# Optimization experiments

Hardware: AMD Instinct MI355X
Metric: run time of the kernel (lower is better)

## Reference

```python
import jax, jax.numpy as jnp
import numpy as np

B, H, W, D = 64, 32, 32, 64
K = 1024  # codebook_size


def setup_inputs() -> dict:
    key = jax.random.key(0)
    kz, ke = jax.random.split(key)
    z = jax.random.normal(kz, (B, H, W, D), dtype=jnp.float32)
    embeddings = 0.02 * jax.random.normal(ke, (K, D), dtype=jnp.float32)
    return {"z": z, "embeddings": embeddings}


def reference(z, embeddings):
    # Flatten spatial/batch dims: (N, D) with N = B*H*W
    z_flat = z.reshape(-1, z.shape[-1])
    # Squared euclidean distances via ||a||^2 + ||b||^2 - 2 a.b  -> (N, K)
    distances = (jnp.sum(z_flat ** 2, axis=1, keepdims=True)
                 + jnp.sum(embeddings ** 2, axis=1)
                 - 2.0 * jnp.dot(z_flat, embeddings.T))
    indices = jnp.argmin(distances, axis=1)  # (N,)
    quantized = embeddings[indices].reshape(z.shape)  # (B, H, W, D)
    indices = indices.reshape(z.shape[0], z.shape[1], z.shape[2])  # (B, H, W)
    return quantized, indices
```

## Files before the change

### kernel.cpp

```cpp
#include <hip/hip_runtime.h>

#define NPTS   65536
#define DDIM   64
#define KCODES 1024
#define QOUT_ELEMS (NPTS * DDIM)

typedef _Float16 half8    __attribute__((ext_vector_type(8)));
typedef float    floatx16 __attribute__((ext_vector_type(16)));
typedef unsigned int uint;

#define AS1 __attribute__((address_space(1)))
#define AS3 __attribute__((address_space(3)))

#define WS_EHP   0
#define WS_ELP   (128*1024)
#define WS_E2    (256*1024)

union H8U { half8 v; uint u[4]; };

static __device__ __forceinline__ void gl_lds16(const void* g, void* l) {
    __builtin_amdgcn_global_load_lds((const AS1 uint*)g, (AS3 uint*)l, 16, 0, 0);
}

__global__ void eprep_kernel(const float* __restrict__ emb, char* __restrict__ ws) {
    const int tid = threadIdx.x;
    const int w = tid >> 6, d = tid & 63;
    const int k = blockIdx.x * 4 + w;
    float v = emb[(size_t)k * DDIM + d];
    _Float16 h = (_Float16)v;
    _Float16 l = (_Float16)(v - (float)h);
    size_t off = (size_t)(k >> 5) * 4096 + (size_t)(d >> 3) * 512
               + (size_t)(k & 31) * 16 + (size_t)(d & 7) * 2;
    *(_Float16*)(ws + WS_EHP + off) = h;
    *(_Float16*)(ws + WS_ELP + off) = l;
    float s = v * v;
    #pragma unroll
    for (int m = 1; m < 64; m <<= 1) s += __shfl_xor(s, m, 64);
    if (d == 0) {
        _Float16 e2h = (_Float16)s;
        _Float16 e2l = (_Float16)(s - (float)e2h);
        unsigned short hb = *(unsigned short*)&e2h;
        unsigned short lb = *(unsigned short*)&e2l;
        ((uint*)(ws + WS_E2))[k] = (uint)hb | ((uint)lb << 16);
    }
}

__global__ __launch_bounds__(256, 3) void vq_kernel(
    const float* __restrict__ z,
    const char* __restrict__ ws_c,
    const float* __restrict__ emb,
    float* __restrict__ out)
{
    const int tid  = threadIdx.x;
    const int lane = tid & 63;
    const int w    = __builtin_amdgcn_readfirstlane(tid >> 6);
    const int col  = lane & 31;
    const int sel8 = lane >> 5;
    const int pgrp = blockIdx.x;

    __shared__ uint4 ldseh[256];
    __shared__ uint4 ldsel[256];
    __shared__ uint  lds_e2[1024];
    __shared__ int   s_final[128];

    const int pt = pgrp * 128 + w * 32 + col;
    half8 ah[4], al[4];
    {
        const float* zrow = z + (size_t)pt * DDIM + sel8 * 8;
        #pragma unroll
        for (int ks = 0; ks < 4; ++ks) {
            float4 u0 = *(const float4*)(zrow + ks * 16);
            float4 u1 = *(const float4*)(zrow + ks * 16 + 4);
            float tv[8] = {u0.x, u0.y, u0.z, u0.w, u1.x, u1.y, u1.z, u1.w};
            #pragma unroll
            for (int j = 0; j < 8; ++j) {
                float a = -2.0f * tv[j];
                _Float16 hh = (_Float16)a;
                ah[ks][j] = hh;
                al[ks][j] = (_Float16)(a - (float)hh);
            }
        }
    }
    half8 ahE;
    { H8U t0; t0.u[0] = (sel8 == 0) ? 0x3C003C00u : 0u;
      t0.u[1] = t0.u[2] = t0.u[3] = 0u; ahE = t0.v; }

    gl_lds16(ws_c + WS_E2 + w * 1024 + lane * 16, (char*)lds_e2 + w * 1024);

    const floatx16 zeroC = {};

    float best[16];
    int   bt[16];
    #pragma unroll
    for (int r = 0; r < 16; ++r) { best[r] = 3.4e38f; bt[r] = 0; }

    const int myoff = sel8 * 512 + col * 16;

    for (int t = 0; t < 32; ++t) {
        __syncthreads();
        {
            const int opnd = w >> 1, half = w & 1;
            const char* src = ws_c + (opnd ? WS_ELP : WS_EHP)
                            + (size_t)t * 4096 + half * 2048 + lane * 16;
            char* dst = (char*)(opnd ? ldsel : ldseh) + half * 2048;
            gl_lds16(src, dst);
            gl_lds16(src + 1024, dst + 1024);
        }
        __syncthreads();

        const char* ehb = (const char*)ldseh + myoff;
        const char* elb = (const char*)ldsel + myoff;
        half8 bh[4], bl[4];
        #pragma unroll
        for (int ks = 0; ks < 4; ++ks) {
            bh[ks] = *(const half8*)(ehb + ks * 1024);
            bl[ks] = *(const half8*)(elb + ks * 1024);
        }
        half8 bhE;
        { H8U u; u.u[0] = lds_e2[t * 32 + col];
          u.u[1] = u.u[2] = u.u[3] = 0u; bhE = u.v; }

        floatx16 acc = __builtin_amdgcn_mfma_f32_32x32x16_f16(ah[0], bh[0], zeroC, 0, 0, 0);
        acc = __builtin_amdgcn_mfma_f32_32x32x16_f16(ah[1], bh[1], acc, 0, 0, 0);
        acc = __builtin_amdgcn_mfma_f32_32x32x16_f16(ah[2], bh[2], acc, 0, 0, 0);
        acc = __builtin_amdgcn_mfma_f32_32x32x16_f16(ah[3], bh[3], acc, 0, 0, 0);
        acc = __builtin_amdgcn_mfma_f32_32x32x16_f16(ahE,  bhE,  acc, 0, 0, 0);
        acc = __builtin_amdgcn_mfma_f32_32x32x16_f16(ah[0], bl[0], acc, 0, 0, 0);
        acc = __builtin_amdgcn_mfma_f32_32x32x16_f16(ah[1], bl[1], acc, 0, 0, 0);
        acc = __builtin_amdgcn_mfma_f32_32x32x16_f16(ah[2], bl[2], acc, 0, 0, 0);
        acc = __builtin_amdgcn_mfma_f32_32x32x16_f16(ah[3], bl[3], acc, 0, 0, 0);
        acc = __builtin_amdgcn_mfma_f32_32x32x16_f16(al[0], bh[0], acc, 0, 0, 0);
        acc = __builtin_amdgcn_mfma_f32_32x32x16_f16(al[1], bh[1], acc, 0, 0, 0);
        acc = __builtin_amdgcn_mfma_f32_32x32x16_f16(al[2], bh[2], acc, 0, 0, 0);
        acc = __builtin_amdgcn_mfma_f32_32x32x16_f16(al[3], bh[3], acc, 0, 0, 0);

        #pragma unroll
        for (int r = 0; r < 16; ++r) {
            bool c = acc[r] < best[r];
            best[r] = c ? acc[r] : best[r];
            bt[r]   = c ? t      : bt[r];
        }
    }

    int code[16];
    #pragma unroll
    for (int r = 0; r < 16; ++r) code[r] = bt[r] * 32 + col;
    #pragma unroll
    for (int m = 1; m < 32; m <<= 1) {
        #pragma unroll
        for (int r = 0; r < 16; ++r) {
            float ov = __shfl_xor(best[r], m, 64);
            int   oc = __shfl_xor(code[r], m, 64);
            bool c = (ov < best[r]) || (ov == best[r] && oc < code[r]);
            best[r] = c ? ov : best[r];
            code[r] = c ? oc : code[r];
        }
    }
    if (col == 0) {
        #pragma unroll
        for (int r = 0; r < 16; ++r) {
            int row = (r & 3) + 8 * (r >> 2) + 4 * sel8;
            s_final[w * 32 + row] = code[r];
        }
    }
    __syncthreads();

    if (tid < 128)
        out[QOUT_ELEMS + (size_t)pgrp * 128 + tid] = (float)s_final[tid];
    float4* outq = (float4*)out;
    const float4* emb4 = (const float4*)emb;
    #pragma unroll
    for (int it = 0; it < 8; ++it) {
        int f  = it * 256 + tid;
        int p  = f >> 4;
        int d4 = f & 15;
        int ks = s_final[p];
        outq[((size_t)pgrp * 128 + p) * (DDIM / 4) + d4] =
            emb4[(size_t)ks * (DDIM / 4) + d4];
    }
}

extern "C" void kernel_launch(void* const* d_in, const int* in_sizes, int n_in,
                              void* d_out, int out_size, void* d_ws, size_t ws_size,
                              hipStream_t stream) {
    const float* z   = (const float*)d_in[0];
    const float* emb = (const float*)d_in[1];
    float* out = (float*)d_out;
    char* ws = (char*)d_ws;

    eprep_kernel<<<KCODES / 4, 256, 0, stream>>>(emb, ws);
    vq_kernel<<<NPTS / 128, 256, 0, stream>>>(z, ws, emb, out);
}
```

Baseline: 102.0 us.

## Split codebook across blocks, double-buffer LDS, add separate merge-gather kernel

Each block now handles 256 points (two 32-row sets per wave) against half the codebook, so every B fragment loaded from LDS feeds two MFMA chains. Codebook tiles are double-buffered in LDS with prefetch, which removes one barrier per iteration. Partial argmins go to a workspace scratch buffer, and a new merge kernel picks between the two halves and does the embedding gather. The cost is a third kernel launch, the scratch round-trip, higher register pressure, and occupancy lowered from 3 to 2 blocks.

```diff
diff --git a/kernel.cpp b/kernel.cpp
--- a/kernel.cpp
+++ b/kernel.cpp
@@ -15,6 +15,7 @@
 #define WS_EHP   0
 #define WS_ELP   (128*1024)
 #define WS_E2    (256*1024)
+#define WS_SCR   (264*1024)
 
 union H8U { half8 v; uint u[4]; };
 
@@ -45,27 +46,26 @@
     }
 }
 
-__global__ __launch_bounds__(256, 3) void vq_kernel(
+__global__ __launch_bounds__(256, 2) void vq_kernel(
     const float* __restrict__ z,
     const char* __restrict__ ws_c,
-    const float* __restrict__ emb,
-    float* __restrict__ out)
+    float2* __restrict__ scr)
 {
     const int tid  = threadIdx.x;
     const int lane = tid & 63;
     const int w    = __builtin_amdgcn_readfirstlane(tid >> 6);
     const int col  = lane & 31;
     const int sel8 = lane >> 5;
-    const int pgrp = blockIdx.x;
-
-    __shared__ uint4 ldseh[256];
-    __shared__ uint4 ldsel[256];
-    __shared__ uint  lds_e2[1024];
-    __shared__ int   s_final[128];
-
-    const int pt = pgrp * 128 + w * 32 + col;
-    half8 ah[4], al[4];
-    {
+    const int pgrp  = blockIdx.x >> 1;
+    const int khalf = blockIdx.x & 1;
+
+    __shared__ uint4 ldsbuf[2][1024];
+    __shared__ uint  lds_e2[512];
+
+    half8 ah[2][4], al[2][4];
+    #pragma unroll
+    for (int set = 0; set < 2; ++set) {
+        const int pt = pgrp * 256 + w * 64 + set * 32 + col;
         const float* zrow = z + (size_t)pt * DDIM + sel8 * 8;
         #pragma unroll
         for (int ks = 0; ks < 4; ++ks) {
@@ -76,8 +76,8 @@
             for (int j = 0; j < 8; ++j) {
                 float a = -2.0f * tv[j];
                 _Float16 hh = (_Float16)a;
-                ah[ks][j] = hh;
-                al[ks][j] = (_Float16)(a - (float)hh);
+                ah[set][ks][j] = hh;
+                al[set][ks][j] = (_Float16)(a - (float)hh);
             }
         }
     }
@@ -85,99 +85,136 @@
     { H8U t0; t0.u[0] = (sel8 == 0) ? 0x3C003C00u : 0u;
       t0.u[1] = t0.u[2] = t0.u[3] = 0u; ahE = t0.v; }
 
-    gl_lds16(ws_c + WS_E2 + w * 1024 + lane * 16, (char*)lds_e2 + w * 1024);
+    if (w < 2)
+        gl_lds16(ws_c + WS_E2 + khalf * 2048 + w * 1024 + lane * 16,
+                 (char*)lds_e2 + w * 1024);
+    {
+        const int opnd = w >> 1, q = w & 1;
+        const char* src = ws_c + (opnd ? WS_ELP : WS_EHP)
+                        + (size_t)(khalf * 16 + q) * 4096 + lane * 16;
+        char* dst = (char*)ldsbuf[0] + (opnd * 8192 + q * 4096);
+        #pragma unroll
+        for (int i = 0; i < 4; ++i)
+            gl_lds16(src + i * 1024, dst + i * 1024);
+    }
 
     const floatx16 zeroC = {};
-
-    float best[16];
-    int   bt[16];
-    #pragma unroll
-    for (int r = 0; r < 16; ++r) { best[r] = 3.4e38f; bt[r] = 0; }
-
-    const int myoff = sel8 * 512 + col * 16;
-
-    for (int t = 0; t < 32; ++t) {
+    float best[2][16];
+    int   bt[2][16];
+    #pragma unroll
+    for (int set = 0; set < 2; ++set)
+        #pragma unroll
+        for (int r = 0; r < 16; ++r) { best[set][r] = 3.4e38f; bt[set][r] = 0; }
+
+    for (int s = 0; s < 8; ++s) {
         __syncthreads();
-        {
-            const int opnd = w >> 1, half = w & 1;
+        if (s < 7) {
+            const int opnd = w >> 1, q = w & 1;
             const char* src = ws_c + (opnd ? WS_ELP : WS_EHP)
-                            + (size_t)t * 4096 + half * 2048 + lane * 16;
-            char* dst = (char*)(opnd ? ldsel : ldseh) + half * 2048;
-            gl_lds16(src, dst);
-            gl_lds16(src + 1024, dst + 1024);
-        }
-        __syncthreads();
-
-        const char* ehb = (const char*)ldseh + myoff;
-        const char* elb = (const char*)ldsel + myoff;
-        half8 bh[4], bl[4];
-        #pragma unroll
-        for (int ks = 0; ks < 4; ++ks) {
-            bh[ks] = *(const half8*)(ehb + ks * 1024);
-            bl[ks] = *(const half8*)(elb + ks * 1024);
-        }
-        half8 bhE;
-        { H8U u; u.u[0] = lds_e2[t * 32 + col];
-          u.u[1] = u.u[2] = u.u[3] = 0u; bhE = u.v; }
-
-        floatx16 acc = __builtin_amdgcn_mfma_f32_32x32x16_f16(ah[0], bh[0], zeroC, 0, 0, 0);
-        acc = __builtin_amdgcn_mfma_f32_32x32x16_f16(ah[1], bh[1], acc, 0, 0, 0);
-        acc = __builtin_amdgcn_mfma_f32_32x32x16_f16(ah[2], bh[2], acc, 0, 0, 0);
-        acc = __builtin_amdgcn_mfma_f32_32x32x16_f16(ah[3], bh[3], acc, 0, 0, 0);
-        acc = __builtin_amdgcn_mfma_f32_32x32x16_f16(ahE,  bhE,  acc, 0, 0, 0);
-        acc = __builtin_amdgcn_mfma_f32_32x32x16_f16(ah[0], bl[0], acc, 0, 0, 0);
-        acc = __builtin_amdgcn_mfma_f32_32x32x16_f16(ah[1], bl[1], acc, 0, 0, 0);
-        acc = __builtin_amdgcn_mfma_f32_32x32x16_f16(ah[2], bl[2], acc, 0, 0, 0);
-        acc = __builtin_amdgcn_mfma_f32_32x32x16_f16(ah[3], bl[3], acc, 0, 0, 0);
-        acc = __builtin_amdgcn_mfma_f32_32x32x16_f16(al[0], bh[0], acc, 0, 0, 0);
-        acc = __builtin_amdgcn_mfma_f32_32x32x16_f16(al[1], bh[1], acc, 0, 0, 0);
-        acc = __builtin_amdgcn_mfma_f32_32x32x16_f16(al[2], bh[2], acc, 0, 0, 0);
-        acc = __builtin_amdgcn_mfma_f32_32x32x16_f16(al[3], bh[3], acc, 0, 0, 0);
-
-        #pragma unroll
-        for (int r = 0; r < 16; ++r) {
-            bool c = acc[r] < best[r];
-            best[r] = c ? acc[r] : best[r];
-            bt[r]   = c ? t      : bt[r];
-        }
-    }
-
-    int code[16];
-    #pragma unroll
-    for (int r = 0; r < 16; ++r) code[r] = bt[r] * 32 + col;
-    #pragma unroll
-    for (int m = 1; m < 32; m <<= 1) {
-        #pragma unroll
-        for (int r = 0; r < 16; ++r) {
-            float ov = __shfl_xor(best[r], m, 64);
-            int   oc = __shfl_xor(code[r], m, 64);
-            bool c = (ov < best[r]) || (ov == best[r] && oc < code[r]);
-            best[r] = c ? ov : best[r];
-            code[r] = c ? oc : code[r];
-        }
-    }
-    if (col == 0) {
-        #pragma unroll
-        for (int r = 0; r < 16; ++r) {
-            int row = (r & 3) + 8 * (r >> 2) + 4 * sel8;
-            s_final[w * 32 + row] = code[r];
-        }
-    }
-    __syncthreads();
-
-    if (tid < 128)
-        out[QOUT_ELEMS + (size_t)pgrp * 128 + tid] = (float)s_final[tid];
-    float4* outq = (float4*)out;
-    const float4* emb4 = (const float4*)emb;
-    #pragma unroll
-    for (int it = 0; it < 8; ++it) {
-        int f  = it * 256 + tid;
-        int p  = f >> 4;
-        int d4 = f & 15;
-        int ks = s_final[p];
-        outq[((size_t)pgrp * 128 + p) * (DDIM / 4) + d4] =
-            emb4[(size_t)ks * (DDIM / 4) + d4];
-    }
+                            + (size_t)(khalf * 16 + (s + 1) * 2 + q) * 4096 + lane * 16;
+            char* dst = (char*)ldsbuf[(s + 1) & 1] + (opnd * 8192 + q * 4096);
+            #pragma unroll
+            for (int i = 0; i < 4; ++i)
+                gl_lds16(src + i * 1024, dst + i * 1024);
+        }
+        const char* buf = (const char*)ldsbuf[s & 1];
+
+        #pragma unroll
+        for (int q = 0; q < 2; ++q) {
+            const int tg = s * 2 + q;
+            const char* ehb = buf + q * 4096 + sel8 * 512 + col * 16;
+            const char* elb = ehb + 8192;
+            half8 bh[4], bl[4];
+            #pragma unroll
+            for (int ks = 0; ks < 4; ++ks) {
+                bh[ks] = *(const half8*)(ehb + ks * 1024);
+                bl[ks] = *(const half8*)(elb + ks * 1024);
+            }
+            half8 bhE;
+            { H8U u; u.u[0] = lds_e2[tg * 32 + col];
+              u.u[1] = u.u[2] = u.u[3] = 0u; bhE = u.v; }
+
+            floatx16 a0, a1;
+            a0 = __builtin_amdgcn_mfma_f32_32x32x16_f16(ah[0][0], bh[0], zeroC, 0, 0, 0);
+            a1 = __builtin_amdgcn_mfma_f32_32x32x16_f16(ah[1][0], bh[0], zeroC, 0, 0, 0);
+            a0 = __builtin_amdgcn_mfma_f32_32x32x16_f16(ah[0][1], bh[1], a0, 0, 0, 0);
+            a1 = __builtin_amdgcn_mfma_f32_32x32x16_f16(ah[1][1], bh[1], a1, 0, 0, 0);
+            a0 = __builtin_amdgcn_mfma_f32_32x32x16_f16(ah[0][2], bh[2], a0, 0, 0, 0);
+            a1 = __builtin_amdgcn_mfma_f32_32x32x16_f16(ah[1][2], bh[2], a1, 0, 0, 0);
+            a0 = __builtin_amdgcn_mfma_f32_32x32x16_f16(ah[0][3], bh[3], a0, 0, 0, 0);
+            a1 = __builtin_amdgcn_mfma_f32_32x32x16_f16(ah[1][3], bh[3], a1, 0, 0, 0);
+            a0 = __builtin_amdgcn_mfma_f32_32x32x16_f16(ahE, bhE, a0, 0, 0, 0);
+            a1 = __builtin_amdgcn_mfma_f32_32x32x16_f16(ahE, bhE, a1, 0, 0, 0);
+            a0 = __builtin_amdgcn_mfma_f32_32x32x16_f16(ah[0][0], bl[0], a0, 0, 0, 0);
+            a1 = __builtin_amdgcn_mfma_f32_32x32x16_f16(ah[1][0], bl[0], a1, 0, 0, 0);
+            a0 = __builtin_amdgcn_mfma_f32_32x32x16_f16(ah[0][1], bl[1], a0, 0, 0, 0);
+            a1 = __builtin_amdgcn_mfma_f32_32x32x16_f16(ah[1][1], bl[1], a1, 0, 0, 0);
+            a0 = __builtin_amdgcn_mfma_f32_32x32x16_f16(ah[0][2], bl[2], a0, 0, 0, 0);
+            a1 = __builtin_amdgcn_mfma_f32_32x32x16_f16(ah[1][2], bl[2], a1, 0, 0, 0);
+            a0 = __builtin_amdgcn_mfma_f32_32x32x16_f16(ah[0][3], bl[3], a0, 0, 0, 0);
+            a1 = __builtin_amdgcn_mfma_f32_32x32x16_f16(ah[1][3], bl[3], a1, 0, 0, 0);
+            a0 = __builtin_amdgcn_mfma_f32_32x32x16_f16(al[0][0], bh[0], a0, 0, 0, 0);
+            a1 = __builtin_amdgcn_mfma_f32_32x32x16_f16(al[1][0], bh[0], a1, 0, 0, 0);
+            a0 = __builtin_amdgcn_mfma_f32_32x32x16_f16(al[0][1], bh[1], a0, 0, 0, 0);
+            a1 = __builtin_amdgcn_mfma_f32_32x32x16_f16(al[1][1], bh[1], a1, 0, 0, 0);
+            a0 = __builtin_amdgcn_mfma_f32_32x32x16_f16(al[0][2], bh[2], a0, 0, 0, 0);
+            a1 = __builtin_amdgcn_mfma_f32_32x32x16_f16(al[1][2], bh[2], a1, 0, 0, 0);
+            a0 = __builtin_amdgcn_mfma_f32_32x32x16_f16(al[0][3], bh[3], a0, 0, 0, 0);
+            a1 = __builtin_amdgcn_mfma_f32_32x32x16_f16(al[1][3], bh[3], a1, 0, 0, 0);
+
+            #pragma unroll
+            for (int r = 0; r < 16; ++r) {
+                bool c0 = a0[r] < best[0][r];
+                best[0][r] = c0 ? a0[r] : best[0][r];
+                bt[0][r]   = c0 ? tg    : bt[0][r];
+                bool c1 = a1[r] < best[1][r];
+                best[1][r] = c1 ? a1[r] : best[1][r];
+                bt[1][r]   = c1 ? tg    : bt[1][r];
+            }
+        }
+    }
+
+    #pragma unroll
+    for (int set = 0; set < 2; ++set) {
+        int code[16];
+        #pragma unroll
+        for (int r = 0; r < 16; ++r)
+            code[r] = khalf * 512 + bt[set][r] * 32 + col;
+        #pragma unroll
+        for (int m = 1; m < 32; m <<= 1) {
+            #pragma unroll
+            for (int r = 0; r < 16; ++r) {
+                float ov = __shfl_xor(best[set][r], m, 64);
+                int   oc = __shfl_xor(code[r], m, 64);
+                bool c = (ov < best[set][r]) || (ov == best[set][r] && oc < code[r]);
+                best[set][r] = c ? ov : best[set][r];
+                code[r]      = c ? oc : code[r];
+            }
+        }
+        if (col == 0) {
+            #pragma unroll
+            for (int r = 0; r < 16; ++r) {
+                int row = (r & 3) + 8 * (r >> 2) + 4 * sel8;
+                int p = pgrp * 256 + w * 64 + set * 32 + row;
+                scr[(size_t)p * 2 + khalf] =
+                    make_float2(best[set][r], __int_as_float(code[r]));
+            }
+        }
+    }
+}
+
+__global__ void merge_gather_kernel(const float* __restrict__ emb,
+                                    const float2* __restrict__ scr,
+                                    float* __restrict__ out)
+{
+    int f = blockIdx.x * 256 + threadIdx.x;
+    int pt = f >> 4, d4 = f & 15;
+    float2 c0 = scr[(size_t)pt * 2];
+    float2 c1 = scr[(size_t)pt * 2 + 1];
+    int i0 = __float_as_int(c0.y), i1 = __float_as_int(c1.y);
+    int idx = (c1.x < c0.x) ? i1 : i0;
+    ((float4*)out)[(size_t)pt * 16 + d4] = ((const float4*)emb)[(size_t)idx * 16 + d4];
+    if (d4 == 0) out[QOUT_ELEMS + pt] = (float)idx;
 }
 
 extern "C" void kernel_launch(void* const* d_in, const int* in_sizes, int n_in,
@@ -187,7 +224,9 @@
     const float* emb = (const float*)d_in[1];
     float* out = (float*)d_out;
     char* ws = (char*)d_ws;
+    float2* scr = (float2*)(ws + WS_SCR);
 
     eprep_kernel<<<KCODES / 4, 256, 0, stream>>>(emb, ws);
-    vq_kernel<<<NPTS / 128, 256, 0, stream>>>(z, ws, emb, out);
-}
+    vq_kernel<<<512, 256, 0, stream>>>(z, ws, scr);
+    merge_gather_kernel<<<NPTS * 16 / 256, 256, 0, stream>>>(emb, scr, out);
+}
```

After: 111.7 us. 1.1x slower.

## Split codebook across 4 blocks per point group with double-buffered LDS and merge kernel

Applied to the files above, without the earlier changes.

Each point group of 128 points is now handled by four blocks, each scanning a quarter of the codebook. That quadruples the grid from 512 to 2048 blocks to fill more CUs. Codebook tiles are double-buffered in LDS, issuing the next tile's load before the current compute, which removes one barrier per iteration. Each block writes partial (best distance, index) pairs to workspace, and a new merge_gather kernel picks the minimum and gathers the embedding rows. The cost is an extra launch, a scratch round-trip, and the z loads and conversion repeated four times. Tie-breaking in the merge keeps the earlier quarter on equal distances, which preserves lowest-index semantics.

```diff
diff --git a/kernel.cpp b/kernel.cpp
--- a/kernel.cpp
+++ b/kernel.cpp
@@ -15,6 +15,7 @@
 #define WS_EHP   0
 #define WS_ELP   (128*1024)
 #define WS_E2    (256*1024)
+#define WS_SCR   (264*1024)
 
 union H8U { half8 v; uint u[4]; };
 
@@ -48,20 +49,18 @@
 __global__ __launch_bounds__(256, 3) void vq_kernel(
     const float* __restrict__ z,
     const char* __restrict__ ws_c,
-    const float* __restrict__ emb,
-    float* __restrict__ out)
+    float2* __restrict__ scr)
 {
     const int tid  = threadIdx.x;
     const int lane = tid & 63;
     const int w    = __builtin_amdgcn_readfirstlane(tid >> 6);
     const int col  = lane & 31;
     const int sel8 = lane >> 5;
-    const int pgrp = blockIdx.x;
-
-    __shared__ uint4 ldseh[256];
-    __shared__ uint4 ldsel[256];
-    __shared__ uint  lds_e2[1024];
-    __shared__ int   s_final[128];
+    const int pgrp = blockIdx.x >> 2;
+    const int kq   = blockIdx.x & 3;
+
+    __shared__ uint4 ldsbuf[2][512];
+    __shared__ uint  lds_e2[256];
 
     const int pt = pgrp * 128 + w * 32 + col;
     half8 ah[4], al[4];
@@ -85,31 +84,36 @@
     { H8U t0; t0.u[0] = (sel8 == 0) ? 0x3C003C00u : 0u;
       t0.u[1] = t0.u[2] = t0.u[3] = 0u; ahE = t0.v; }
 
-    gl_lds16(ws_c + WS_E2 + w * 1024 + lane * 16, (char*)lds_e2 + w * 1024);
+    if (w == 0)
+        gl_lds16(ws_c + WS_E2 + kq * 1024 + lane * 16, (char*)lds_e2);
+    {
+        const int opnd = w >> 1, hf = w & 1;
+        const char* src = ws_c + (opnd ? WS_ELP : WS_EHP)
+                        + (size_t)(kq * 8) * 4096 + hf * 2048 + lane * 16;
+        char* dst = (char*)ldsbuf[0] + opnd * 4096 + hf * 2048;
+        gl_lds16(src, dst);
+        gl_lds16(src + 1024, dst + 1024);
+    }
 
     const floatx16 zeroC = {};
-
     float best[16];
     int   bt[16];
     #pragma unroll
     for (int r = 0; r < 16; ++r) { best[r] = 3.4e38f; bt[r] = 0; }
 
-    const int myoff = sel8 * 512 + col * 16;
-
-    for (int t = 0; t < 32; ++t) {
+    for (int t = 0; t < 8; ++t) {
         __syncthreads();
-        {
-            const int opnd = w >> 1, half = w & 1;
+        if (t < 7) {
+            const int opnd = w >> 1, hf = w & 1;
             const char* src = ws_c + (opnd ? WS_ELP : WS_EHP)
-                            + (size_t)t * 4096 + half * 2048 + lane * 16;
-            char* dst = (char*)(opnd ? ldsel : ldseh) + half * 2048;
+                            + (size_t)(kq * 8 + t + 1) * 4096 + hf * 2048 + lane * 16;
+            char* dst = (char*)ldsbuf[(t + 1) & 1] + opnd * 4096 + hf * 2048;
             gl_lds16(src, dst);
             gl_lds16(src + 1024, dst + 1024);
         }
-        __syncthreads();
-
-        const char* ehb = (const char*)ldseh + myoff;
-        const char* elb = (const char*)ldsel + myoff;
+        const char* buf = (const char*)ldsbuf[t & 1];
+        const char* ehb = buf + sel8 * 512 + col * 16;
+        const char* elb = ehb + 4096;
         half8 bh[4], bl[4];
         #pragma unroll
         for (int ks = 0; ks < 4; ++ks) {
@@ -120,7 +124,8 @@
         { H8U u; u.u[0] = lds_e2[t * 32 + col];
           u.u[1] = u.u[2] = u.u[3] = 0u; bhE = u.v; }
 
-        floatx16 acc = __builtin_amdgcn_mfma_f32_32x32x16_f16(ah[0], bh[0], zeroC, 0, 0, 0);
+        floatx16 acc;
+        acc = __builtin_amdgcn_mfma_f32_32x32x16_f16(ah[0], bh[0], zeroC, 0, 0, 0);
         acc = __builtin_amdgcn_mfma_f32_32x32x16_f16(ah[1], bh[1], acc, 0, 0, 0);
         acc = __builtin_amdgcn_mfma_f32_32x32x16_f16(ah[2], bh[2], acc, 0, 0, 0);
         acc = __builtin_amdgcn_mfma_f32_32x32x16_f16(ah[3], bh[3], acc, 0, 0, 0);
@@ -144,7 +149,7 @@
 
     int code[16];
     #pragma unroll
-    for (int r = 0; r < 16; ++r) code[r] = bt[r] * 32 + col;
+    for (int r = 0; r < 16; ++r) code[r] = kq * 256 + bt[r] * 32 + col;
     #pragma unroll
     for (int m = 1; m < 32; m <<= 1) {
         #pragma unroll
@@ -160,24 +165,27 @@
         #pragma unroll
         for (int r = 0; r < 16; ++r) {
             int row = (r & 3) + 8 * (r >> 2) + 4 * sel8;
-            s_final[w * 32 + row] = code[r];
-        }
-    }
-    __syncthreads();
-
-    if (tid < 128)
-        out[QOUT_ELEMS + (size_t)pgrp * 128 + tid] = (float)s_final[tid];
-    float4* outq = (float4*)out;
-    const float4* emb4 = (const float4*)emb;
-    #pragma unroll
-    for (int it = 0; it < 8; ++it) {
-        int f  = it * 256 + tid;
-        int p  = f >> 4;
-        int d4 = f & 15;
-        int ks = s_final[p];
-        outq[((size_t)pgrp * 128 + p) * (DDIM / 4) + d4] =
-            emb4[(size_t)ks * (DDIM / 4) + d4];
-    }
+            int p = pgrp * 128 + w * 32 + row;
+            scr[(size_t)p * 4 + kq] = make_float2(best[r], __int_as_float(code[r]));
+        }
+    }
+}
+
+__global__ void merge_gather_kernel(const float* __restrict__ emb,
+                                    const float2* __restrict__ scr,
+                                    float* __restrict__ out)
+{
+    int f = blockIdx.x * 256 + threadIdx.x;
+    int pt = f >> 4, d4 = f & 15;
+    float2 c0 = scr[(size_t)pt * 4];
+    float bv = c0.x; int bi = __float_as_int(c0.y);
+    #pragma unroll
+    for (int j = 1; j < 4; ++j) {
+        float2 cj = scr[(size_t)pt * 4 + j];
+        if (cj.x < bv) { bv = cj.x; bi = __float_as_int(cj.y); }
+    }
+    ((float4*)out)[(size_t)pt * 16 + d4] = ((const float4*)emb)[(size_t)bi * 16 + d4];
+    if (d4 == 0) out[QOUT_ELEMS + pt] = (float)bi;
 }
 
 extern "C" void kernel_launch(void* const* d_in, const int* in_sizes, int n_in,
@@ -187,7 +195,9 @@
     const float* emb = (const float*)d_in[1];
     float* out = (float*)d_out;
     char* ws = (char*)d_ws;
+    float2* scr = (float2*)(ws + WS_SCR);
 
     eprep_kernel<<<KCODES / 4, 256, 0, stream>>>(emb, ws);
-    vq_kernel<<<NPTS / 128, 256, 0, stream>>>(z, ws, emb, out);
-}
+    vq_kernel<<<2048, 256, 0, stream>>>(z, ws, scr);
+    merge_gather_kernel<<<NPTS * 16 / 256, 256, 0, stream>>>(emb, scr, out);
+}
```

After: 118.0 us. 1.16x slower.

## Use single-wave blocks with register double-buffered codebook loads from global memory

Applied to the files above, without the earlier changes.

Replaces the 4-wave block that staged codebook tiles through LDS with barriers with 64-thread single-wave blocks. Each wave loads B-operand tiles straight from global memory (L2-cached) into registers, double-buffered so the next tile's load overlaps the current tile's MFMAs. The ||e||^2 term is now added in fp32 after the MFMAs instead of through an extra MFMA. The gather epilogue is also done per wave without LDS. This removes the barriers and the LDS traffic, but every wave now re-reads the whole codebook from global/L2, which raises cache bandwidth pressure.

```diff
diff --git a/kernel.cpp b/kernel.cpp
--- a/kernel.cpp
+++ b/kernel.cpp
@@ -9,18 +9,9 @@
 typedef float    floatx16 __attribute__((ext_vector_type(16)));
 typedef unsigned int uint;
 
-#define AS1 __attribute__((address_space(1)))
-#define AS3 __attribute__((address_space(3)))
-
 #define WS_EHP   0
 #define WS_ELP   (128*1024)
-#define WS_E2    (256*1024)
-
-union H8U { half8 v; uint u[4]; };
-
-static __device__ __forceinline__ void gl_lds16(const void* g, void* l) {
-    __builtin_amdgcn_global_load_lds((const AS1 uint*)g, (AS3 uint*)l, 16, 0, 0);
-}
+#define WS_E2F   (256*1024)
 
 __global__ void eprep_kernel(const float* __restrict__ emb, char* __restrict__ ws) {
     const int tid = threadIdx.x;
@@ -36,37 +27,58 @@
     float s = v * v;
     #pragma unroll
     for (int m = 1; m < 64; m <<= 1) s += __shfl_xor(s, m, 64);
-    if (d == 0) {
-        _Float16 e2h = (_Float16)s;
-        _Float16 e2l = (_Float16)(s - (float)e2h);
-        unsigned short hb = *(unsigned short*)&e2h;
-        unsigned short lb = *(unsigned short*)&e2l;
-        ((uint*)(ws + WS_E2))[k] = (uint)hb | ((uint)lb << 16);
-    }
+    if (d == 0) ((float*)(ws + WS_E2F))[k] = s;
 }
 
-__global__ __launch_bounds__(256, 3) void vq_kernel(
+#define MFMA __builtin_amdgcn_mfma_f32_32x32x16_f16
+
+#define LOAD_TILE(BH, BL, E2V, tt) do {                                       \
+    const char* _p = ws_c + WS_EHP + (size_t)(tt) * 4096 + sel8 * 512 + col * 16; \
+    _Pragma("unroll") for (int _k = 0; _k < 4; ++_k)                          \
+        BH[_k] = *(const half8*)(_p + _k * 1024);                             \
+    _Pragma("unroll") for (int _k = 0; _k < 4; ++_k)                          \
+        BL[_k] = *(const half8*)(_p + (WS_ELP - WS_EHP) + _k * 1024);         \
+    E2V = e2f[(tt) * 32 + col];                                               \
+} while (0)
+
+#define DO_TILE(BH, BL, E2V, TCUR) do {                                       \
+    floatx16 acc;                                                             \
+    acc = MFMA(ah[0], BH[0], zeroC, 0, 0, 0);                                 \
+    acc = MFMA(ah[1], BH[1], acc, 0, 0, 0);                                   \
+    acc = MFMA(ah[2], BH[2], acc, 0, 0, 0);                                   \
+    acc = MFMA(ah[3], BH[3], acc, 0, 0, 0);                                   \
+    acc = MFMA(ah[0], BL[0], acc, 0, 0, 0);                                   \
+    acc = MFMA(ah[1], BL[1], acc, 0, 0, 0);                                   \
+    acc = MFMA(ah[2], BL[2], acc, 0, 0, 0);                                   \
+    acc = MFMA(ah[3], BL[3], acc, 0, 0, 0);                                   \
+    acc = MFMA(al[0], BH[0], acc, 0, 0, 0);                                   \
+    acc = MFMA(al[1], BH[1], acc, 0, 0, 0);                                   \
+    acc = MFMA(al[2], BH[2], acc, 0, 0, 0);                                   \
+    acc = MFMA(al[3], BH[3], acc, 0, 0, 0);                                   \
+    const int vcode = (TCUR) * 32 + col;                                      \
+    _Pragma("unroll") for (int _r = 0; _r < 16; ++_r) {                       \
+        float _s = acc[_r] + (E2V);                                           \
+        bool _c = _s < best[_r];        \
+        best[_r]  = _c ? _s    : best[_r];                                    \
+        bcode[_r] = _c ? vcode : bcode[_r];                                   \
+    }                                                                         \
+} while (0)
+
+__global__ __launch_bounds__(64, 2) void vq_kernel(
     const float* __restrict__ z,
     const char* __restrict__ ws_c,
     const float* __restrict__ emb,
     float* __restrict__ out)
 {
-    const int tid  = threadIdx.x;
-    const int lane = tid & 63;
-    const int w    = __builtin_amdgcn_readfirstlane(tid >> 6);
+    const int lane = threadIdx.x & 63;
     const int col  = lane & 31;
     const int sel8 = lane >> 5;
-    const int pgrp = blockIdx.x;
+    const int ptbase = blockIdx.x * 32;
+    const float* e2f = (const float*)(ws_c + WS_E2F);
 
-    __shared__ uint4 ldseh[256];
-    __shared__ uint4 ldsel[256];
-    __shared__ uint  lds_e2[1024];
-    __shared__ int   s_final[128];
-
-    const int pt = pgrp * 128 + w * 32 + col;
     half8 ah[4], al[4];
     {
-        const float* zrow = z + (size_t)pt * DDIM + sel8 * 8;
+        const float* zrow = z + (size_t)(ptbase + col) * DDIM + sel8 * 8;
         #pragma unroll
         for (int ks = 0; ks < 4; ++ks) {
             float4 u0 = *(const float4*)(zrow + ks * 16);
@@ -81,102 +93,44 @@
             }
         }
     }
-    half8 ahE;
-    { H8U t0; t0.u[0] = (sel8 == 0) ? 0x3C003C00u : 0u;
-      t0.u[1] = t0.u[2] = t0.u[3] = 0u; ahE = t0.v; }
-
-    gl_lds16(ws_c + WS_E2 + w * 1024 + lane * 16, (char*)lds_e2 + w * 1024);
 
     const floatx16 zeroC = {};
+    float best[16];
+    int   bcode[16];
+    #pragma unroll
+    for (int r = 0; r < 16; ++r) { best[r] = 3.4e38f; bcode[r] = 0; }
 
-    float best[16];
-    int   bt[16];
-    #pragma unroll
-    for (int r = 0; r < 16; ++r) { best[r] = 3.4e38f; bt[r] = 0; }
-
-    const int myoff = sel8 * 512 + col * 16;
-
-    for (int t = 0; t < 32; ++t) {
-        __syncthreads();
-        {
-            const int opnd = w >> 1, half = w & 1;
-            const char* src = ws_c + (opnd ? WS_ELP : WS_EHP)
-                            + (size_t)t * 4096 + half * 2048 + lane * 16;
-            char* dst = (char*)(opnd ? ldsel : ldseh) + half * 2048;
-            gl_lds16(src, dst);
-            gl_lds16(src + 1024, dst + 1024);
-        }
-        __syncthreads();
-
-        const char* ehb = (const char*)ldseh + myoff;
-        const char* elb = (const char*)ldsel + myoff;
-        half8 bh[4], bl[4];
-        #pragma unroll
-        for (int ks = 0; ks < 4; ++ks) {
-            bh[ks] = *(const half8*)(ehb + ks * 1024);
-            bl[ks] = *(const half8*)(elb + ks * 1024);
-        }
-        half8 bhE;
-        { H8U u; u.u[0] = lds_e2[t * 32 + col];
-          u.u[1] = u.u[2] = u.u[3] = 0u; bhE = u.v; }
-
-        floatx16 acc = __builtin_amdgcn_mfma_f32_32x32x16_f16(ah[0], bh[0], zeroC, 0, 0, 0);
-        acc = __builtin_amdgcn_mfma_f32_32x32x16_f16(ah[1], bh[1], acc, 0, 0, 0);
-        acc = __builtin_amdgcn_mfma_f32_32x32x16_f16(ah[2], bh[2], acc, 0, 0, 0);
-        acc = __builtin_amdgcn_mfma_f32_32x32x16_f16(ah[3], bh[3], acc, 0, 0, 0);
-        acc = __builtin_amdgcn_mfma_f32_32x32x16_f16(ahE,  bhE,  acc, 0, 0, 0);
-        acc = __builtin_amdgcn_mfma_f32_32x32x16_f16(ah[0], bl[0], acc, 0, 0, 0);
-        acc = __builtin_amdgcn_mfma_f32_32x32x16_f16(ah[1], bl[1], acc, 0, 0, 0);
-        acc = __builtin_amdgcn_mfma_f32_32x32x16_f16(ah[2], bl[2], acc, 0, 0, 0);
-        acc = __builtin_amdgcn_mfma_f32_32x32x16_f16(ah[3], bl[3], acc, 0, 0, 0);
-        acc = __builtin_amdgcn_mfma_f32_32x32x16_f16(al[0], bh[0], acc, 0, 0, 0);
-        acc = __builtin_amdgcn_mfma_f32_32x32x16_f16(al[1], bh[1], acc, 0, 0, 0);
-        acc = __builtin_amdgcn_mfma_f32_32x32x16_f16(al[2], bh[2], acc, 0, 0, 0);
-        acc = __builtin_amdgcn_mfma_f32_32x32x16_f16(al[3], bh[3], acc, 0, 0, 0);
-
-        #pragma unroll
-        for (int r = 0; r < 16; ++r) {
-            bool c = acc[r] < best[r];
-            best[r] = c ? acc[r] : best[r];
-            bt[r]   = c ? t      : bt[r];
-        }
+    half8 b0h[4], b0l[4], b1h[4], b1l[4];
+    float e20, e21;
+    LOAD_TILE(b0h, b0l, e20, 0);
+    for (int t = 0; t < 32; t += 2) {
+        LOAD_TILE(b1h, b1l, e21, t + 1);
+        DO_TILE(b0h, b0l, e20, t);
+        const int t2 = (t + 2 < 32) ? t + 2 : 31;
+        LOAD_TILE(b0h, b0l, e20, t2);
+        DO_TILE(b1h, b1l, e21, t + 1);
     }
 
-    int code[16];
-    #pragma unroll
-    for (int r = 0; r < 16; ++r) code[r] = bt[r] * 32 + col;
     #pragma unroll
     for (int m = 1; m < 32; m <<= 1) {
         #pragma unroll
         for (int r = 0; r < 16; ++r) {
-            float ov = __shfl_xor(best[r], m, 64);
-            int   oc = __shfl_xor(code[r], m, 64);
-            bool c = (ov < best[r]) || (ov == best[r] && oc < code[r]);
-            best[r] = c ? ov : best[r];
-            code[r] = c ? oc : code[r];
+            float ov = __shfl_xor(best[r],  m, 64);
+            int   oc = __shfl_xor(bcode[r], m, 64);
+            bool c = (ov < best[r]) || (ov == best[r] && oc < bcode[r]);
+            best[r]  = c ? ov : best[r];
+            bcode[r] = c ? oc : bcode[r];
         }
     }
-    if (col == 0) {
-        #pragma unroll
-        for (int r = 0; r < 16; ++r) {
-            int row = (r & 3) + 8 * (r >> 2) + 4 * sel8;
-            s_final[w * 32 + row] = code[r];
-        }
-    }
-    __syncthreads();
 
-    if (tid < 128)
-        out[QOUT_ELEMS + (size_t)pgrp * 128 + tid] = (float)s_final[tid];
-    float4* outq = (float4*)out;
-    const float4* emb4 = (const float4*)emb;
     #pragma unroll
-    for (int it = 0; it < 8; ++it) {
-        int f  = it * 256 + tid;
-        int p  = f >> 4;
-        int d4 = f & 15;
-        int ks = s_final[p];
-        outq[((size_t)pgrp * 128 + p) * (DDIM / 4) + d4] =
-            emb4[(size_t)ks * (DDIM / 4) + d4];
+    for (int r = 0; r < 16; ++r) {
+        int row = (r & 3) + 8 * (r >> 2) + 4 * sel8;
+        int p = ptbase + row;
+        int code = bcode[r];
+        float2 v = ((const float2*)emb)[(size_t)code * 32 + col];
+        ((float2*)out)[(size_t)p * 32 + col] = v;
+        if (col == 0) out[QOUT_ELEMS + p] = (float)code;
     }
 }
 
@@ -189,5 +143,5 @@
     char* ws = (char*)d_ws;
 
     eprep_kernel<<<KCODES / 4, 256, 0, stream>>>(emb, ws);
-    vq_kernel<<<NPTS / 128, 256, 0, stream>>>(z, ws, emb, out);
+    vq_kernel<<<NPTS / 32, 64, 0, stream>>>(z, ws, emb, out);
 }
```

Result: slower. 125.7 us (+23.2%).
